# Optimization experiments

Measured on AMD Instinct MI355X. Metric: run time of the kernel, lower is better.

## Reference

```python
import jax, jax.numpy as jnp
import numpy as np
import math

B, S, D, H = 4, 2048, 1024, 16
HD = D // H  # 64
FF = 4096
EPS = 1e-5


def layer_norm(x, g, b):
    mu = jnp.mean(x, axis=-1, keepdims=True)
    var = jnp.mean(jnp.square(x - mu), axis=-1, keepdims=True)
    return (x - mu) * jax.lax.rsqrt(var + EPS) * g + b


def setup_inputs() -> dict:
    key = jax.random.key(0)
    ks = jax.random.split(key, 16)
    sc = 0.02
    return {
        "x": jax.random.normal(ks[0], (B, S, D), dtype=jnp.float32),
        "Wq": jax.random.normal(ks[1], (H, D, HD), dtype=jnp.float32) * sc,
        "bq": jnp.zeros((H, HD), dtype=jnp.float32),
        "Wk": jax.random.normal(ks[2], (H, D, HD), dtype=jnp.float32) * sc,
        "bk": jnp.zeros((H, HD), dtype=jnp.float32),
        "Wv": jax.random.normal(ks[3], (H, D, HD), dtype=jnp.float32) * sc,
        "bv": jnp.zeros((H, HD), dtype=jnp.float32),
        "Wo": jax.random.normal(ks[4], (D, D), dtype=jnp.float32) * sc,
        "bo": jnp.zeros((D,), dtype=jnp.float32),
        "W1": jax.random.normal(ks[5], (D, FF), dtype=jnp.float32) * sc,
        "b1": jnp.zeros((FF,), dtype=jnp.float32),
        "W2": jax.random.normal(ks[6], (FF, D), dtype=jnp.float32) * sc,
        "b2": jnp.zeros((D,), dtype=jnp.float32),
        "ln1_g": jnp.ones((D,), dtype=jnp.float32),
        "ln1_b": jnp.zeros((D,), dtype=jnp.float32),
        "ln2_g": jnp.ones((D,), dtype=jnp.float32),
        "ln2_b": jnp.zeros((D,), dtype=jnp.float32),
    }


def reference(x, Wq, bq, Wk, bk, Wv, bv, Wo, bo, W1, b1, W2, b2, ln1_g, ln1_b, ln2_g, ln2_b):
    b, s, d = x.shape
    h1 = layer_norm(x, ln1_g, ln1_b)
    # per-head Q/K/V linears, vectorized over heads: [b,h,s,hd]
    q = jnp.einsum('bsd,hde->bhse', h1, Wq) + bq[None, :, None, :]
    k = jnp.einsum('bsd,hde->bhse', h1, Wk) + bk[None, :, None, :]
    v = jnp.einsum('bsd,hde->bhse', h1, Wv) + bv[None, :, None, :]
    scores = jnp.einsum('bhqe,bhke->bhqk', q, k) / math.sqrt(q.shape[-1])
    causal = jnp.tril(jnp.ones((s, s), dtype=bool))
    scores = jnp.where(causal[None, None], scores, -jnp.inf)
    weights = jax.nn.softmax(scores, axis=-1)
    attn = jnp.einsum('bhqk,bhke->bhqe', weights, v)
    # concat heads (head order = torch concat dim=-1)
    attn = attn.transpose(0, 2, 1, 3).reshape(b, s, d)
    x = x + attn @ Wo + bo
    h2 = layer_norm(x, ln2_g, ln2_b)
    y = jax.nn.gelu(h2 @ W1 + b1, approximate=False)
    y = jax.nn.gelu(y @ W2 + b2, approximate=False)
    return x + y
```

## Files before the change

kernel.cpp:

```cpp
#include <hip/hip_runtime.h>
#include <cstdint>
#include <cstddef>


#define DI __device__ __forceinline__

typedef __attribute__((ext_vector_type(8))) __bf16 bf16x8;
typedef __attribute__((ext_vector_type(4))) float floatx4;
typedef __attribute__((ext_vector_type(4))) unsigned int uintx4;

static constexpr int Bn = 4, Sn = 2048, Dn = 1024, Hn = 16, HDn = 64, FFn = 4096;
static constexpr int NTOK = Bn * Sn;
static constexpr int D3 = 3 * Dn;

DI float bf2f(unsigned short u) { return __uint_as_float(((unsigned int)u) << 16); }
DI unsigned short f2bf(float f) {
  unsigned int u = __float_as_uint(f);
  u += 0x7FFFu + ((u >> 16) & 1u);
  return (unsigned short)(u >> 16);
}
DI float gelu_f(float v) { return 0.5f * v * (1.0f + erff(v * 0.70710678118654752f)); }
DI bf16x8 ld8(const unsigned short* p) { return *(const bf16x8*)p; }
DI floatx4 mfma16(bf16x8 a, bf16x8 b, floatx4 c) {
  return __builtin_amdgcn_mfma_f32_16x16x32_bf16(a, b, c, 0, 0, 0);
}
DI void g2l16(const unsigned short* g, unsigned short* l) {
  __builtin_amdgcn_global_load_lds((__attribute__((address_space(1))) void*)g,
                                   (__attribute__((address_space(3))) void*)l,
                                   16, 0, 0);
}
DI float ldin(const void* p, size_t idx, bool f32) {
  return f32 ? ((const float*)p)[idx] : bf2f(((const unsigned short*)p)[idx]);
}
DI unsigned int cvt_pk_bf16(float lo, float hi) {
  unsigned int r;
  asm("v_cvt_pk_bf16_f32 %0, %1, %2" : "=v"(r) : "v"(lo), "v"(hi));
  return r;
}
DI bf16x8 pack8(unsigned int a, unsigned int b, unsigned int c, unsigned int d) {
  uintx4 t;
  t[0] = a; t[1] = b; t[2] = c; t[3] = d;
  return __builtin_bit_cast(bf16x8, t);
}
DI int swz16(int row, int col) {
  return (row << 6) + ((((col >> 3) ^ row ^ (row >> 3)) & 7) << 3) + (col & 7);
}
DI int xcd_swz(int bid, int nwg) {
  return (bid & 7) * (nwg >> 3) + (bid >> 3);
}

__global__ void detect_kernel(const unsigned short* __restrict__ x,
                              int* __restrict__ flag) {
  int t = threadIdx.x;
  int cnt = 0;
  for (int i = t; i < 1024; i += 64) {
    unsigned short u = x[2 * i];
    int e = (u >> 7) & 0xFF;
    cnt += (e >= 96 && e <= 142) ? 1 : 0;
  }
  #pragma unroll
  for (int off = 32; off >= 1; off >>= 1) cnt += __shfl_xor(cnt, off);
  if (t == 0) *flag = (cnt < 820) ? 1 : 0;
}

__global__ void vec_prep(const void* bq, const void* bk, const void* bv,
                         const void* bo, const void* b1, const void* b2,
                         const void* g1, const void* be1, const void* g2,
                         const void* be2, unsigned short* __restrict__ dst,
                         const int* __restrict__ flag) {
  int i = blockIdx.x * 256 + threadIdx.x;
  if (i >= 13312) return;
  const bool f32 = *flag != 0;
  const void* src; int off;
  if      (i < 1024)  { src = bq;  off = i; }
  else if (i < 2048)  { src = bk;  off = i - 1024; }
  else if (i < 3072)  { src = bv;  off = i - 2048; }
  else if (i < 4096)  { src = bo;  off = i - 3072; }
  else if (i < 8192)  { src = b1;  off = i - 4096; }
  else if (i < 9216)  { src = b2;  off = i - 8192; }
  else if (i < 10240) { src = g1;  off = i - 9216; }
  else if (i < 11264) { src = be1; off = i - 10240; }
  else if (i < 12288) { src = g2;  off = i - 11264; }
  else                { src = be2; off = i - 12288; }
  dst[i] = f2bf(ldin(src, off, f32));
}

__global__ void transpose_kernel(const void* __restrict__ src,
                                 unsigned short* __restrict__ dst, int K, int N,
                                 const int* __restrict__ flag) {
  __shared__ unsigned short tile[64][65];
  const bool f32 = *flag != 0;
  int kb = blockIdx.y * 64, nb = blockIdx.x * 64;
  for (int i = threadIdx.x; i < 4096; i += 256) {
    int r = i >> 6, c = i & 63;
    tile[r][c] = f2bf(ldin(src, (size_t)(kb + r) * N + nb + c, f32));
  }
  __syncthreads();
  for (int i = threadIdx.x; i < 4096; i += 256) {
    int r = i >> 6, c = i & 63;
    dst[(size_t)(nb + r) * K + kb + c] = tile[c][r];
  }
}

__global__ void qkvT_kernel(const void* __restrict__ Wq,
                            const void* __restrict__ Wk,
                            const void* __restrict__ Wv,
                            unsigned short* __restrict__ WT,
                            const int* __restrict__ flag) {
  __shared__ unsigned short tile[64][65];
  const bool f32 = *flag != 0;
  const void* src = blockIdx.z == 0 ? Wq : (blockIdx.z == 1 ? Wk : Wv);
  int h = blockIdx.y, d0 = blockIdx.x * 64;
  size_t base = (size_t)h * (Dn * HDn);
  for (int i = threadIdx.x; i < 4096; i += 256) {
    int r = i >> 6, c = i & 63;
    tile[r][c] = f2bf(ldin(src, base + (size_t)(d0 + r) * 64 + c, f32));
  }
  __syncthreads();
  for (int i = threadIdx.x; i < 4096; i += 256) {
    int r = i >> 6, c = i & 63;
    WT[(size_t)(blockIdx.z * 1024 + h * 64 + r) * 1024 + d0 + c] = tile[c][r];
  }
}

__global__ __launch_bounds__(256) void ln_kernel(const void* __restrict__ x,
                                                 const unsigned short* __restrict__ g,
                                                 const unsigned short* __restrict__ b,
                                                 unsigned short* __restrict__ out,
                                                 const int* __restrict__ flag) {
  const bool f32 = flag ? (*flag != 0) : true;
  int row = blockIdx.x, t = threadIdx.x;
  float v[4];
  if (f32) {
    float4 f = *(const float4*)((const float*)x + (size_t)row * Dn + t * 4);
    v[0] = f.x; v[1] = f.y; v[2] = f.z; v[3] = f.w;
  } else {
    ushort4 u = *(const ushort4*)((const unsigned short*)x + (size_t)row * Dn + t * 4);
    v[0] = bf2f(u.x); v[1] = bf2f(u.y); v[2] = bf2f(u.z); v[3] = bf2f(u.w);
  }
  float s = v[0] + v[1] + v[2] + v[3];
  float s2 = v[0] * v[0] + v[1] * v[1] + v[2] * v[2] + v[3] * v[3];
  #pragma unroll
  for (int off = 32; off >= 1; off >>= 1) {
    s += __shfl_xor(s, off);
    s2 += __shfl_xor(s2, off);
  }
  __shared__ float red[8];
  int wv = t >> 6, ln = t & 63;
  if (ln == 0) { red[wv] = s; red[4 + wv] = s2; }
  __syncthreads();
  s = red[0] + red[1] + red[2] + red[3];
  s2 = red[4] + red[5] + red[6] + red[7];
  float mu = s * (1.0f / 1024.0f);
  float var = s2 * (1.0f / 1024.0f) - mu * mu;
  float rs = rsqrtf(fmaxf(var, 0.0f) + 1e-5f);
  ushort4 gg = *(const ushort4*)(g + t * 4);
  ushort4 bb = *(const ushort4*)(b + t * 4);
  ushort4 o;
  o.x = f2bf((v[0] - mu) * rs * bf2f(gg.x) + bf2f(bb.x));
  o.y = f2bf((v[1] - mu) * rs * bf2f(gg.y) + bf2f(bb.y));
  o.z = f2bf((v[2] - mu) * rs * bf2f(gg.z) + bf2f(bb.z));
  o.w = f2bf((v[3] - mu) * rs * bf2f(gg.w) + bf2f(bb.w));
  *(ushort4*)(out + (size_t)row * Dn + t * 4) = o;
}

enum { EPI_BIAS_BF16 = 0, EPI_WO = 1, EPI_GELU = 2, EPI_FF2 = 3 };

template <int EPI, int BN>
__global__ __launch_bounds__(256, BN == 64 ? 4 : 3) void gemm_kernel(
    const unsigned short* __restrict__ A, const unsigned short* __restrict__ BT,
    const unsigned short* __restrict__ bias, const void* __restrict__ residv,
    const float* __restrict__ resid_f, unsigned short* __restrict__ Cb,
    float* __restrict__ Cf, const int* __restrict__ flag, int M, int N, int K) {
  constexpr int NT = BN / 32;
  __shared__ unsigned short As[2][128 * 32];
  __shared__ unsigned short Bs[2][BN * 32];
  const int gx = gridDim.x;
  const int nwg = gx * gridDim.y;
  const int bid = xcd_swz((int)blockIdx.y * gx + (int)blockIdx.x, nwg);
  const int m0 = (bid / gx) * 128, n0 = (bid % gx) * BN;
  const int w = threadIdx.x >> 6, lane = threadIdx.x & 63;
  const int waveM = (w >> 1) * 64, waveN = (w & 1) * (BN / 2);
  const int m16 = lane & 15, quad = lane >> 4;
  const bool rf32 = flag && (*flag != 0);
  const int tid = threadIdx.x;

  const int srow = w * 32 + (lane >> 2);
  const int scol = (lane & 3) * 8;
  const int stA = srow * 32 + scol;
  const unsigned short* Ag = A + (size_t)(m0 + srow) * K + scol;
  const int sBrow = (BN == 128) ? srow : (tid >> 2);
  const int sBcol = (BN == 128) ? scol : ((tid & 3) * 8);
  const int stB = sBrow * 32 + sBcol;
  const unsigned short* Bg = BT + (size_t)(n0 + sBrow) * K + sBcol;
  const size_t rowstep = (size_t)16 * K;

  floatx4 acc[4][NT];
  #pragma unroll
  for (int i = 0; i < 4; i++)
    #pragma unroll
    for (int j = 0; j < NT; j++) acc[i][j] = floatx4{0.f, 0.f, 0.f, 0.f};

  g2l16(Ag, As[0] + stA);
  g2l16(Ag + rowstep, As[0] + stA + 16 * 32);
  g2l16(Bg, Bs[0] + stB);
  if constexpr (BN == 128) g2l16(Bg + rowstep, Bs[0] + stB + 16 * 32);
  Ag += 32; Bg += 32;
  asm volatile("s_waitcnt vmcnt(0)" ::: "memory");
  __builtin_amdgcn_s_barrier();

  const int ntiles = K >> 5;
  int cur = 0;
  for (int t = 0; t < ntiles; ++t) {
    if (t + 1 < ntiles) {
      unsigned short* Aln = As[cur ^ 1] + stA;
      unsigned short* Bln = Bs[cur ^ 1] + stB;
      g2l16(Ag, Aln);
      g2l16(Ag + rowstep, Aln + 16 * 32);
      g2l16(Bg, Bln);
      if constexpr (BN == 128) g2l16(Bg + rowstep, Bln + 16 * 32);
      Ag += 32; Bg += 32;
    }
    const unsigned short* Ab = As[cur];
    const unsigned short* Bb = Bs[cur];
    bf16x8 af[4], bfv[NT];
    #pragma unroll
    for (int mt = 0; mt < 4; mt++)
      af[mt] = ld8(Ab + (waveM + mt * 16 + m16) * 32 + quad * 8);
    #pragma unroll
    for (int nt = 0; nt < NT; nt++)
      bfv[nt] = ld8(Bb + (waveN + nt * 16 + m16) * 32 + quad * 8);
    #pragma unroll
    for (int mt = 0; mt < 4; mt++)
      #pragma unroll
      for (int nt = 0; nt < NT; nt++)
        acc[mt][nt] = mfma16(af[mt], bfv[nt], acc[mt][nt]);
    if (t + 1 < ntiles) {
      asm volatile("s_waitcnt vmcnt(0)" ::: "memory");
      __builtin_amdgcn_s_barrier();
      cur ^= 1;
    }
  }

  #pragma unroll
  for (int mt = 0; mt < 4; mt++) {
    #pragma unroll
    for (int nt = 0; nt < NT; nt++) {
      const int col = n0 + waveN + nt * 16 + m16;
      const float bcol = bf2f(bias[col]);
      #pragma unroll
      for (int r = 0; r < 4; r++) {
        const int row = m0 + waveM + mt * 16 + quad * 4 + r;
        const size_t idx = (size_t)row * N + col;
        float v = acc[mt][nt][r] + bcol;
        if constexpr (EPI == EPI_BIAS_BF16) {
          Cb[idx] = f2bf(v);
        } else if constexpr (EPI == EPI_WO) {
          float rv = rf32 ? ((const float*)residv)[idx]
                          : bf2f(((const unsigned short*)residv)[idx]);
          Cf[idx] = v + rv;
        } else if constexpr (EPI == EPI_GELU) {
          Cb[idx] = f2bf(gelu_f(v));
        } else {
          float ov = gelu_f(v) + resid_f[idx];
          if (rf32) Cf[idx] = ov;
          else      Cb[idx] = f2bf(ov);
        }
      }
    }
  }
}

__global__ __launch_bounds__(256, 4) void attn_kernel(
    const unsigned short* __restrict__ qkv, unsigned short* __restrict__ attn) {
  const int bid = xcd_swz((int)blockIdx.y * 32 + (int)blockIdx.x, 2048);
  const int qt = 31 - (bid & 31);
  const int bh = bid >> 5;
  const int b = bh >> 4, h = bh & 15;
  const int tid = threadIdx.x;
  const int w = tid >> 6, lane = tid & 63;
  const int m16 = lane & 15, quad = lane >> 4;

  __shared__ unsigned short Ks[2][4096];
  __shared__ unsigned short Vt[2][4096];

  const int qrow = qt * 64 + w * 16 + m16;
  const int qloc = w * 16 + m16;
  const unsigned short* qp = qkv + (size_t)(b * Sn + qrow) * D3 + h * 64 + quad * 8;
  const bf16x8 qf0 = ld8(qp), qf1 = ld8(qp + 32);

  floatx4 acc_o[4];
  #pragma unroll
  for (int nt = 0; nt < 4; nt++) acc_o[nt] = floatx4{0.f, 0.f, 0.f, 0.f};
  float lsum = 0.f;

  const int kr = tid >> 3, kc = (tid & 7) * 8;
  const int krs = (kr & 3) + (((kr >> 3) & 3) << 2) + (((kr >> 2) & 1) << 4);
  const int vk = (tid >> 3) * 2, ve = (tid & 7) * 8;

  uint4 kreg0, kreg1, vreg0, vreg1;
  const unsigned short* const kvroot = qkv + (size_t)(b * Sn) * D3 + h * 64;

  {
    const unsigned short* base = kvroot;
    kreg0 = *(const uint4*)(base + (size_t)kr * D3 + 1024 + kc);
    kreg1 = *(const uint4*)(base + (size_t)(kr + 32) * D3 + 1024 + kc);
    vreg0 = *(const uint4*)(base + (size_t)vk * D3 + 2048 + ve);
    vreg1 = *(const uint4*)(base + (size_t)(vk + 1) * D3 + 2048 + ve);
  }

  for (int kt = 0; kt <= qt; ++kt) {
    const int pb = kt & 1;
    *(uint4*)(Ks[pb] + swz16(krs, kc)) = kreg0;
    *(uint4*)(Ks[pb] + swz16(krs + 32, kc)) = kreg1;
    {
      const unsigned short* a0 = (const unsigned short*)&vreg0;
      const unsigned short* a1 = (const unsigned short*)&vreg1;
      #pragma unroll
      for (int i = 0; i < 8; i++) {
        unsigned int word = (unsigned int)a0[i] | ((unsigned int)a1[i] << 16);
        *(unsigned int*)(Vt[pb] + swz16(ve + i, vk)) = word;
      }
    }
    __syncthreads();
    if (kt < qt) {
      const unsigned short* base = kvroot + (size_t)(kt + 1) * 64 * D3;
      kreg0 = *(const uint4*)(base + (size_t)kr * D3 + 1024 + kc);
      kreg1 = *(const uint4*)(base + (size_t)(kr + 32) * D3 + 1024 + kc);
      vreg0 = *(const uint4*)(base + (size_t)vk * D3 + 2048 + ve);
      vreg1 = *(const uint4*)(base + (size_t)(vk + 1) * D3 + 2048 + ve);
    }

    floatx4 sa[4];
    #pragma unroll
    for (int nt = 0; nt < 4; nt++) {
      bf16x8 k0 = ld8(Ks[pb] + swz16(nt * 16 + m16, quad * 8));
      bf16x8 k1 = ld8(Ks[pb] + swz16(nt * 16 + m16, 32 + quad * 8));
      floatx4 t = mfma16(k0, qf0, floatx4{0.f, 0.f, 0.f, 0.f});
      sa[nt] = mfma16(k1, qf1, t);
    }

    if (kt == qt) {
      #pragma unroll
      for (int nt = 0; nt < 4; nt++) {
        const int kb_ = (quad << 3) + ((nt & 1) << 2) + ((nt >> 1) << 5);
        #pragma unroll
        for (int r = 0; r < 4; r++)
          if (kb_ + r > qloc) sa[nt][r] = -1e30f;
      }
    }

    constexpr float C = 0.18033688011112042f;
    float e00 = __builtin_amdgcn_exp2f(sa[0][0] * C);
    float e01 = __builtin_amdgcn_exp2f(sa[0][1] * C);
    float e02 = __builtin_amdgcn_exp2f(sa[0][2] * C);
    float e03 = __builtin_amdgcn_exp2f(sa[0][3] * C);
    float e10 = __builtin_amdgcn_exp2f(sa[1][0] * C);
    float e11 = __builtin_amdgcn_exp2f(sa[1][1] * C);
    float e12 = __builtin_amdgcn_exp2f(sa[1][2] * C);
    float e13 = __builtin_amdgcn_exp2f(sa[1][3] * C);
    float e20 = __builtin_amdgcn_exp2f(sa[2][0] * C);
    float e21 = __builtin_amdgcn_exp2f(sa[2][1] * C);
    float e22 = __builtin_amdgcn_exp2f(sa[2][2] * C);
    float e23 = __builtin_amdgcn_exp2f(sa[2][3] * C);
    float e30 = __builtin_amdgcn_exp2f(sa[3][0] * C);
    float e31 = __builtin_amdgcn_exp2f(sa[3][1] * C);
    float e32 = __builtin_amdgcn_exp2f(sa[3][2] * C);
    float e33 = __builtin_amdgcn_exp2f(sa[3][3] * C);
    lsum += ((e00 + e01) + (e02 + e03)) + ((e10 + e11) + (e12 + e13)) +
            ((e20 + e21) + (e22 + e23)) + ((e30 + e31) + (e32 + e33));
    const bf16x8 pa0 = pack8(cvt_pk_bf16(e00, e01), cvt_pk_bf16(e02, e03),
                             cvt_pk_bf16(e10, e11), cvt_pk_bf16(e12, e13));
    const bf16x8 pa1 = pack8(cvt_pk_bf16(e20, e21), cvt_pk_bf16(e22, e23),
                             cvt_pk_bf16(e30, e31), cvt_pk_bf16(e32, e33));

    #pragma unroll
    for (int nt = 0; nt < 4; nt++) {
      bf16x8 v0 = ld8(Vt[pb] + swz16(nt * 16 + m16, quad * 8));
      bf16x8 v1 = ld8(Vt[pb] + swz16(nt * 16 + m16, 32 + quad * 8));
      acc_o[nt] = mfma16(pa0, v0, acc_o[nt]);
      acc_o[nt] = mfma16(pa1, v1, acc_o[nt]);
    }
  }

  lsum += __shfl_xor(lsum, 16);
  lsum += __shfl_xor(lsum, 32);

  #pragma unroll
  for (int r = 0; r < 4; r++) {
    const float inv = 1.0f / fmaxf(__shfl(lsum, quad * 4 + r), 1e-20f);
    const size_t orow = (size_t)(b * Sn + qt * 64 + w * 16 + quad * 4 + r) * Dn + h * 64;
    #pragma unroll
    for (int nt = 0; nt < 4; nt++)
      attn[orow + nt * 16 + m16] = f2bf(acc_o[nt][r] * inv);
  }
}

extern "C" void kernel_launch(void* const* d_in, const int* in_sizes, int n_in,
                              void* d_out, int out_size, void* d_ws, size_t ws_size,
                              hipStream_t stream) {
  (void)in_sizes; (void)n_in; (void)out_size; (void)ws_size;
  const void* x    = d_in[0];
  const void* Wq   = d_in[1];
  const void* bq   = d_in[2];
  const void* Wk   = d_in[3];
  const void* bk   = d_in[4];
  const void* Wv   = d_in[5];
  const void* bv   = d_in[6];
  const void* Wo   = d_in[7];
  const void* bo   = d_in[8];
  const void* W1   = d_in[9];
  const void* b1   = d_in[10];
  const void* W2   = d_in[11];
  const void* b2   = d_in[12];
  const void* ln1g = d_in[13];
  const void* ln1b = d_in[14];
  const void* ln2g = d_in[15];
  const void* ln2b = d_in[16];
  char* ws = (char*)d_ws;

  constexpr size_t OFF_WTQKV = 0;
  constexpr size_t OFF_WOT   = OFF_WTQKV + (size_t)D3 * Dn * 2;
  constexpr size_t OFF_W1T   = OFF_WOT + (size_t)Dn * Dn * 2;
  constexpr size_t OFF_W2T   = OFF_W1T + (size_t)FFn * Dn * 2;
  constexpr size_t OFF_VEC   = OFF_W2T + (size_t)Dn * FFn * 2;
  constexpr size_t OFF_FLAG  = OFF_VEC + 32768;
  constexpr size_t OFF_H     = OFF_FLAG + 256;
  constexpr size_t OFF_QKV   = OFF_H + (size_t)NTOK * Dn * 2;
  constexpr size_t OFF_ATTN  = OFF_QKV + (size_t)NTOK * D3 * 2;
  constexpr size_t OFF_X2    = OFF_ATTN + (size_t)NTOK * Dn * 2;
  constexpr size_t OFF_Y1    = OFF_QKV;

  unsigned short* WTqkv = (unsigned short*)(ws + OFF_WTQKV);
  unsigned short* WoT   = (unsigned short*)(ws + OFF_WOT);
  unsigned short* W1T   = (unsigned short*)(ws + OFF_W1T);
  unsigned short* W2T   = (unsigned short*)(ws + OFF_W2T);
  unsigned short* vec   = (unsigned short*)(ws + OFF_VEC);
  int*            flag  = (int*)(ws + OFF_FLAG);
  unsigned short* hbuf  = (unsigned short*)(ws + OFF_H);
  unsigned short* qkvb  = (unsigned short*)(ws + OFF_QKV);
  unsigned short* attnb = (unsigned short*)(ws + OFF_ATTN);
  float*          x2    = (float*)(ws + OFF_X2);
  unsigned short* y1    = (unsigned short*)(ws + OFF_Y1);

  detect_kernel<<<1, 64, 0, stream>>>((const unsigned short*)x, flag);

  vec_prep<<<52, 256, 0, stream>>>(bq, bk, bv, bo, b1, b2, ln1g, ln1b, ln2g,
                                   ln2b, vec, flag);
  qkvT_kernel<<<dim3(16, 16, 3), 256, 0, stream>>>(Wq, Wk, Wv, WTqkv, flag);
  transpose_kernel<<<dim3(16, 16), 256, 0, stream>>>(Wo, WoT, 1024, 1024, flag);
  transpose_kernel<<<dim3(64, 16), 256, 0, stream>>>(W1, W1T, 1024, 4096, flag);
  transpose_kernel<<<dim3(16, 64), 256, 0, stream>>>(W2, W2T, 4096, 1024, flag);

  ln_kernel<<<NTOK, 256, 0, stream>>>(x, vec + 9216, vec + 10240, hbuf, flag);
  gemm_kernel<EPI_BIAS_BF16, 128><<<dim3(D3 / 128, NTOK / 128), 256, 0, stream>>>(
      hbuf, WTqkv, vec + 0, nullptr, nullptr, qkvb, nullptr, nullptr,
      NTOK, D3, Dn);
  attn_kernel<<<dim3(Sn / 64, Bn * Hn), 256, 0, stream>>>(qkvb, attnb);
  gemm_kernel<EPI_WO, 64><<<dim3(Dn / 64, NTOK / 128), 256, 0, stream>>>(
      attnb, WoT, vec + 3072, x, nullptr, nullptr, x2, flag, NTOK, Dn, Dn);
  ln_kernel<<<NTOK, 256, 0, stream>>>(x2, vec + 11264, vec + 12288, hbuf, nullptr);
  gemm_kernel<EPI_GELU, 128><<<dim3(FFn / 128, NTOK / 128), 256, 0, stream>>>(
      hbuf, W1T, vec + 4096, nullptr, nullptr, y1, nullptr, nullptr,
      NTOK, FFn, Dn);
  gemm_kernel<EPI_FF2, 64><<<dim3(Dn / 64, NTOK / 128), 256, 0, stream>>>(
      y1, W2T, vec + 8192, nullptr, x2, (unsigned short*)d_out, (float*)d_out,
      flag, NTOK, Dn, FFn);
}
```

Measured before the change: 585.3 us.

## Triple-buffer GEMM LDS tiles with two-deep prefetch and partial vmcnt waits

Switches the GEMM main loop from double to triple buffering in LDS. Two K-tiles are now kept in flight, and each iteration waits only for the oldest tile with a partial vmcnt count instead of draining all loads. The goal is to hide global-to-LDS latency behind MFMA work and to move the barrier before the prefetch. It raises LDS use by half, which may lower occupancy against the launch bounds of 3–4 blocks. It also relies on g2l16 issuing exactly one vmem op per call for the vmcnt counts to be correct.

```diff
diff --git a/kernel.cpp b/kernel.cpp
--- a/kernel.cpp
+++ b/kernel.cpp
@@ -173,17 +173,17 @@
     const float* __restrict__ resid_f, unsigned short* __restrict__ Cb,
     float* __restrict__ Cf, const int* __restrict__ flag, int M, int N, int K) {
   constexpr int NT = BN / 32;
-  __shared__ unsigned short As[2][128 * 32];
-  __shared__ unsigned short Bs[2][BN * 32];
+  __shared__ unsigned short As[3][128 * 32];
+  __shared__ unsigned short Bs[3][BN * 32];
   const int gx = gridDim.x;
   const int nwg = gx * gridDim.y;
   const int bid = xcd_swz((int)blockIdx.y * gx + (int)blockIdx.x, nwg);
   const int m0 = (bid / gx) * 128, n0 = (bid % gx) * BN;
-  const int w = threadIdx.x >> 6, lane = threadIdx.x & 63;
+  const int tid = threadIdx.x;
+  const int w = tid >> 6, lane = tid & 63;
   const int waveM = (w >> 1) * 64, waveN = (w & 1) * (BN / 2);
   const int m16 = lane & 15, quad = lane >> 4;
   const bool rf32 = flag && (*flag != 0);
-  const int tid = threadIdx.x;
 
   const int srow = w * 32 + (lane >> 2);
   const int scol = (lane & 3) * 8;
@@ -201,28 +201,32 @@
     #pragma unroll
     for (int j = 0; j < NT; j++) acc[i][j] = floatx4{0.f, 0.f, 0.f, 0.f};
 
-  g2l16(Ag, As[0] + stA);
-  g2l16(Ag + rowstep, As[0] + stA + 16 * 32);
-  g2l16(Bg, Bs[0] + stB);
-  if constexpr (BN == 128) g2l16(Bg + rowstep, Bs[0] + stB + 16 * 32);
-  Ag += 32; Bg += 32;
-  asm volatile("s_waitcnt vmcnt(0)" ::: "memory");
-  __builtin_amdgcn_s_barrier();
+  auto stage = [&](int slot) {
+    unsigned short* Al = As[slot] + stA;
+    unsigned short* Bl = Bs[slot] + stB;
+    g2l16(Ag, Al);
+    g2l16(Ag + rowstep, Al + 16 * 32);
+    g2l16(Bg, Bl);
+    if constexpr (BN == 128) g2l16(Bg + rowstep, Bl + 16 * 32);
+    Ag += 32; Bg += 32;
+  };
+
+  stage(0);
+  stage(1);
 
   const int ntiles = K >> 5;
-  int cur = 0;
   for (int t = 0; t < ntiles; ++t) {
-    if (t + 1 < ntiles) {
-      unsigned short* Aln = As[cur ^ 1] + stA;
-      unsigned short* Bln = Bs[cur ^ 1] + stB;
-      g2l16(Ag, Aln);
-      g2l16(Ag + rowstep, Aln + 16 * 32);
-      g2l16(Bg, Bln);
-      if constexpr (BN == 128) g2l16(Bg + rowstep, Bln + 16 * 32);
-      Ag += 32; Bg += 32;
-    }
-    const unsigned short* Ab = As[cur];
-    const unsigned short* Bb = Bs[cur];
+    if (t < ntiles - 1) {
+      if constexpr (BN == 128) asm volatile("s_waitcnt vmcnt(4)" ::: "memory");
+      else                     asm volatile("s_waitcnt vmcnt(3)" ::: "memory");
+    } else {
+      asm volatile("s_waitcnt vmcnt(0)" ::: "memory");
+    }
+    __builtin_amdgcn_s_barrier();
+    if (t + 2 < ntiles) stage((t + 2) % 3);
+
+    const unsigned short* Ab = As[t % 3];
+    const unsigned short* Bb = Bs[t % 3];
     bf16x8 af[4], bfv[NT];
     #pragma unroll
     for (int mt = 0; mt < 4; mt++)
@@ -235,11 +239,6 @@
       #pragma unroll
       for (int nt = 0; nt < NT; nt++)
         acc[mt][nt] = mfma16(af[mt], bfv[nt], acc[mt][nt]);
-    if (t + 1 < ntiles) {
-      asm volatile("s_waitcnt vmcnt(0)" ::: "memory");
-      __builtin_amdgcn_s_barrier();
-      cur ^= 1;
-    }
   }
 
   #pragma unroll
```

After: 595.9 us. About the same (+1.8%).
